# Performance work log

Measured on AMD Instinct MI355X. Metric: run time of the kernel, lower is better.

## Reference

```python
import jax, jax.numpy as jnp
import numpy as np

INPUT_DIM = 256
DEPTH = 8
HIDDEN = 64
NUM_INNER = 2 ** DEPTH - 1   # 255
NUM_LEAVES = 2 ** DEPTH      # 256
BATCH = 8192


def _xavier(key, shape, fan_in, fan_out):
    bound = jnp.sqrt(6.0 / (fan_in + fan_out)).astype(jnp.float32)
    return jax.random.uniform(key, shape, jnp.float32, -bound, bound)


def setup_inputs() -> dict:
    key = jax.random.key(0)
    k = jax.random.split(key, 5)
    x = jax.random.normal(k[0], (BATCH, INPUT_DIM), jnp.float32)
    # Batched per-node MLP params (one slice per inner node)
    w1 = _xavier(k[1], (NUM_INNER, HIDDEN, INPUT_DIM), INPUT_DIM, HIDDEN)
    b1 = jnp.zeros((NUM_INNER, HIDDEN), jnp.float32)
    w2 = _xavier(k[2], (NUM_INNER, HIDDEN), HIDDEN, 1)
    b2 = jnp.zeros((NUM_INNER,), jnp.float32)
    leaf = _xavier(k[3], (NUM_LEAVES, 1), NUM_LEAVES, 1)
    return {"x": x, "w1": w1, "b1": b1, "w2": w2, "b2": b2, "leaf": leaf}


def reference(x, w1, b1, w2, b2, leaf):
    B = x.shape[0]
    # Fused per-node MLPs: hidden [B, N, H]
    h = jax.nn.relu(jnp.einsum("bi,nhi->bnh", x, w1) + b1)
    logits = jnp.einsum("bnh,nh->bn", h, w2) + b2        # [B, N]
    node_outputs = jax.nn.sigmoid(logits)                 # p, in BFS node order

    # Tree traversal: level-by-level interleave. Child of node j at a level
    # are 2j (left, weight 1-p) and 2j+1 (right, weight p) at the next level.
    reach_levels = []
    cur = jnp.ones((B, 1), x.dtype)
    for level in range(DEPTH):
        reach_levels.append(cur)
        lo = (1 << level) - 1
        p_lvl = node_outputs[:, lo : lo + (1 << level)]   # [B, 2^level]
        cur = jnp.stack([cur * (1.0 - p_lvl), cur * p_lvl], axis=-1).reshape(B, -1)
    node_reach = jnp.concatenate(reach_levels, axis=1)    # [B, NUM_INNER], BFS order
    path_probs = cur                                      # [B, NUM_LEAVES]

    h_out = (path_probs @ leaf)[:, 0]                     # [B]
    return h_out, path_probs, node_outputs, node_reach
```

## Files before the change

kernel.cpp:

```cpp
#include <hip/hip_runtime.h>
#include <cstdint>

#define BATCH   8192
#define KDIM    256
#define HID     64
#define NODES   255
#define NPG     16

typedef unsigned short u16;
typedef unsigned int u32;
typedef short bf16x8 __attribute__((ext_vector_type(8)));
typedef float f32x16 __attribute__((ext_vector_type(16)));


__device__ __forceinline__ u32 f2bf(float f) {
  u32 u = __float_as_uint(f);
  return (u + 0x7FFFu + ((u >> 16) & 1u)) >> 16;
}

__device__ __forceinline__ void gld_lds16(const void* g, void* l) {
  typedef __attribute__((address_space(1))) void* gp_t;
  typedef __attribute__((address_space(3))) void* lp_t;
  gp_t gp = reinterpret_cast<gp_t>(reinterpret_cast<uintptr_t>(g));
  lp_t lp = reinterpret_cast<lp_t>(static_cast<u32>(reinterpret_cast<uintptr_t>(l)));
  __builtin_amdgcn_global_load_lds(gp, lp, 16, 0, 0);
}


#define NPRM 16320

__global__ __launch_bounds__(256) void cvt_kernel(
    const float* __restrict__ x, const float* __restrict__ w1,
    const float* __restrict__ b1, const float* __restrict__ w2,
    u16* __restrict__ xpack, u16* __restrict__ w1pk,
    float* __restrict__ b1p, float* __restrict__ w2p) {
  const int tid = threadIdx.x;
  const int blk = blockIdx.x;

  if (blk < 256) {
    __shared__ u16 sT[32 * 268];
    const float* xs = x + (size_t)blk * 32 * KDIM;
#pragma unroll
    for (int j = 0; j < 8; ++j) {
      int idx = j * 256 + tid;
      float4 v = ((const float4*)xs)[idx];
      int row = idx >> 6, f4 = idx & 63;
      *(u32*)&sT[row * 268 + f4 * 4]     = f2bf(v.x) | (f2bf(v.y) << 16);
      *(u32*)&sT[row * 268 + f4 * 4 + 2] = f2bf(v.z) | (f2bf(v.w) << 16);
    }
    __syncthreads();
#pragma unroll
    for (int j = 0; j < 4; ++j) {
      int d = j * 256 + tid;
      int ks = d >> 6, hl = (d >> 5) & 1, l31 = d & 31;
      const u16* s8 = &sT[l31 * 268 + ks * 16 + hl * 8];
      u32 a = *(const u32*)s8, b = *(const u32*)(s8 + 2);
      u32 c = *(const u32*)(s8 + 4), e = *(const u32*)(s8 + 6);
      uint4 o = {a, b, c, e};
      ((uint4*)xpack)[(size_t)blk * 1024 + d] = o;
    }
  } else if (blk < 511) {
    __shared__ u16 sT[64 * 260];
    const int node = blk - 256;
    const float* src = w1 + (size_t)node * (HID * KDIM);
#pragma unroll
    for (int r = 0; r < 16; ++r) {
      int idx = r * 256 + tid;
      float4 v = ((const float4*)src)[idx];
      int h = idx >> 6, f4 = idx & 63;
      uint2 o;
      o.x = f2bf(v.x) | (f2bf(v.y) << 16);
      o.y = f2bf(v.z) | (f2bf(v.w) << 16);
      *(uint2*)&sT[h * 260 + f4 * 4] = o;
    }
    __syncthreads();
    u16* dst = w1pk + (size_t)node * (HID * KDIM);
#pragma unroll
    for (int r = 0; r < 8; ++r) {
      int g = r * 256 + tid;
      int kb = g >> 6, h = g & 63;
      const u16* s8 = &sT[h * 260 + kb * 8];
      uint2 lo = *(const uint2*)s8;
      uint2 hi = *(const uint2*)(s8 + 4);
      uint4 o = {lo.x, lo.y, hi.x, hi.y};
      ((uint4*)dst)[g] = o;
    }
  } else {
    int i2 = (blk - 511) * 256 + tid;
    if (i2 < 2 * NPRM) {
      int a = i2 >= NPRM;
      int j = a ? i2 - NPRM : i2;
      int reg = j & 15, rt = (j >> 4) & 1, hl = (j >> 5) & 1, node = j >> 6;
      int h = rt * 32 + (reg & 3) + 8 * (reg >> 2) + 4 * hl;
      float v = (a ? b1 : w2)[node * 64 + h];
      (a ? b1p : w2p)[j] = v;
    }
  }
}


__global__ __launch_bounds__(256, 2) void fused_mlp_kernel(
    const u16* __restrict__ xpack,
    const u16* __restrict__ w1pk,
    const float* __restrict__ b1p,
    const float* __restrict__ w2p,
    const float* __restrict__ b2,
    float* __restrict__ no_t)
{
  __shared__ __align__(16) u16 sW[2][16384];
  __shared__ __align__(16) float sW2[NPG * 64];
  __shared__ __align__(16) float sB1[NPG * 64];
  __shared__ float sP[2][4][64];

  const int tid  = threadIdx.x;
  const int lane = tid & 63;
  const int wv   = tid >> 6;
  const int l31  = lane & 31;
  const int hl   = lane >> 5;
  const int rt   = wv & 1;
  const int ch   = wv >> 1;
  const int nbase = blockIdx.y * NPG;

  auto stage_node = [&](int nodeIdx, int bufIdx) {
    const u16* base = w1pk + (size_t)nodeIdx * (HID * KDIM);
    char* lb = (char*)(&sW[bufIdx][0]);
#pragma unroll
    for (int j = 0; j < 8; ++j) {
      int s = j * 256 + tid;
      gld_lds16(base + s * 8, lb + s * 16);
    }
  };

  stage_node(nbase, 0);
  gld_lds16(w2p + (size_t)nbase * 64 + tid * 4, (char*)sW2 + tid * 16);
  gld_lds16(b1p + (size_t)nbase * 64 + tid * 4, (char*)sB1 + tid * 16);

  const int ctile0 = blockIdx.x * 4 + ch * 2;
  bf16x8 xf[2][16];
#pragma unroll
  for (int ct = 0; ct < 2; ++ct) {
    const u16* src = xpack + ((size_t)(ctile0 + ct) * 16) * 512 + lane * 8;
#pragma unroll
    for (int ks = 0; ks < 16; ++ks)
      xf[ct][ks] = *(const bf16x8*)(src + ks * 512);
  }

  const u32 abase = (u32)(hl * 64 + rt * 32 + l31) * 16u;

  __syncthreads();
  int buf = 0, par = 0;

  for (int i = 0; i < NPG; ++i) {
    const int node = nbase + i;

    if (i + 1 < NPG) stage_node(nbase + i + 1, buf ^ 1);

    f32x16 acc0 = (f32x16){0}, acc1 = (f32x16){0};
    const char* sw = (const char*)&sW[buf][0] + abase;
#pragma unroll
    for (int ks = 0; ks < 16; ++ks) {
      bf16x8 a = *(const bf16x8*)(sw + ks * 2048);
      acc0 = __builtin_amdgcn_mfma_f32_32x32x16_bf16(a, xf[0][ks], acc0, 0, 0, 0);
      acc1 = __builtin_amdgcn_mfma_f32_32x32x16_bf16(a, xf[1][ks], acc1, 0, 0, 0);
    }

    float p0 = 0.f, p1 = 0.f;
#pragma unroll
    for (int qd = 0; qd < 4; ++qd) {
      int o = i * 64 + hl * 32 + rt * 16 + qd * 4;
      float4 wq = *(const float4*)&sW2[o];
      float4 bq = *(const float4*)&sB1[o];
#pragma unroll
      for (int e = 0; e < 4; ++e) {
        float w = (&wq.x)[e];
        float bb = (&bq.x)[e];
        p0 += fmaxf(acc0[qd * 4 + e] + bb, 0.f) * w;
        p1 += fmaxf(acc1[qd * 4 + e] + bb, 0.f) * w;
      }
    }
    p0 += __shfl_xor(p0, 32);
    p1 += __shfl_xor(p1, 32);
    if (hl == 0) {
      sP[par][wv][l31]      = p0;
      sP[par][wv][32 + l31] = p1;
    }

    __syncthreads();

    if (tid < 128 && node < NODES) {
      int chh = tid >> 6, c = tid & 63;
      float logit = sP[par][chh * 2][c] + sP[par][chh * 2 + 1][c] + b2[node];
      float sig = 1.0f / (1.0f + expf(-logit));
      no_t[(size_t)node * BATCH + blockIdx.x * 128 + tid] = sig;
    }

    buf ^= 1;
    par ^= 1;
  }
}


__global__ __launch_bounds__(256) void tree_kernel(
    const float* __restrict__ no_t,
    const float* __restrict__ leaf,
    float* __restrict__ out)
{
  __shared__ float p[16][257];

  const int tid = threadIdx.x;
  const int bbase = blockIdx.x * 16;
  const int wave = tid >> 6;
  const int lane = tid & 63;

  for (int i = tid; i < NODES * 16; i += 256) {
    int n = i >> 4, r = i & 15;
    p[r][n] = no_t[(size_t)n * BATCH + bbase + r];
  }
  __syncthreads();

  float4 lw = ((const float4*)leaf)[lane];

  float* h_out  = out;
  float* pp_out = out + 8192;
  float* no_out = out + 8192 + 8192 * 256;
  float* nr_out = out + 8192 + 8192 * 256 + 8192 * (size_t)NODES;

  for (int j = 0; j < 4; ++j) {
    const int r = wave * 4 + j;
    const int b = bbase + r;
    const float* pr = p[r];
    float* nr_b = nr_out + (size_t)b * NODES;

    float rc = 1.f;
#pragma unroll
    for (int L = 0; L < 6; ++L) {
      if (lane < (1 << L)) nr_b[(1 << L) - 1 + lane] = rc;
      float par = __shfl(rc, lane >> 1);
      float pv = pr[(1 << L) - 1 + (lane >> 1)];
      rc = par * ((lane & 1) ? pv : (1.f - pv));
    }
    nr_b[63 + lane] = rc;
    float p6 = pr[63 + lane];
    float r7a = rc * (1.f - p6), r7b = rc * p6;
    nr_b[127 + 2 * lane]     = r7a;
    nr_b[127 + 2 * lane + 1] = r7b;
    float p7a = pr[127 + 2 * lane], p7b = pr[127 + 2 * lane + 1];
    float4 pp;
    pp.x = r7a * (1.f - p7a);
    pp.y = r7a * p7a;
    pp.z = r7b * (1.f - p7b);
    pp.w = r7b * p7b;
    ((float4*)(pp_out + (size_t)b * 256))[lane] = pp;

    float* no_b = no_out + (size_t)b * NODES;
#pragma unroll
    for (int k = 0; k < 4; ++k) {
      int n = lane + 64 * k;
      if (n < NODES) no_b[n] = pr[n];
    }

    float hacc = pp.x * lw.x + pp.y * lw.y + pp.z * lw.z + pp.w * lw.w;
    hacc += __shfl_xor(hacc, 1);
    hacc += __shfl_xor(hacc, 2);
    hacc += __shfl_xor(hacc, 4);
    hacc += __shfl_xor(hacc, 8);
    hacc += __shfl_xor(hacc, 16);
    hacc += __shfl_xor(hacc, 32);
    if (lane == 0) h_out[b] = hacc;
  }
}


extern "C" void kernel_launch(void* const* d_in, const int* in_sizes, int n_in,
                              void* d_out, int out_size, void* d_ws, size_t ws_size,
                              hipStream_t stream) {
  const float* x    = (const float*)d_in[0];
  const float* w1   = (const float*)d_in[1];
  const float* b1   = (const float*)d_in[2];
  const float* w2   = (const float*)d_in[3];
  const float* b2   = (const float*)d_in[4];
  const float* leaf = (const float*)d_in[5];
  float* out = (float*)d_out;

  char* ws = (char*)d_ws;
  u16*   xpack = (u16*)ws;
  u16*   w1pk  = (u16*)(ws + (size_t)4194304);
  float* w2p   = (float*)(ws + (size_t)12582912);
  float* b1p   = (float*)(ws + (size_t)12648192);
  float* no_t  = (float*)(ws + (size_t)12713472);

  cvt_kernel<<<639, 256, 0, stream>>>(x, w1, b1, w2, xpack, w1pk, b1p, w2p);

  dim3 g(64, 16);
  fused_mlp_kernel<<<g, 256, 0, stream>>>(xpack, w1pk, b1p, w2p, b2, no_t);

  tree_kernel<<<BATCH / 16, 256, 0, stream>>>(no_t, leaf, out);
}
```

Measured before the change: 157.5 us.

## Compute full hidden dimension per wave and drop cross-wave LDS reduction

Each wave now computes all 64 hidden rows of a node for its own 64 batch columns, using four MFMA accumulators instead of two. Previously two waves each handled half the hidden rows and combined partial logits through shared memory. The change removes that LDS reduction and lets every thread write the sigmoid output directly. Each block now covers 256 batch rows, so the grid halves and each staged W1 tile is reused across twice as many columns. The cost is higher accumulator register pressure and half as many blocks to spread across the GPU.

```diff
diff --git a/kernel.cpp b/kernel.cpp
--- a/kernel.cpp
+++ b/kernel.cpp
@@ -110,15 +110,12 @@
   __shared__ __align__(16) u16 sW[2][16384];
   __shared__ __align__(16) float sW2[NPG * 64];
   __shared__ __align__(16) float sB1[NPG * 64];
-  __shared__ float sP[2][4][64];
 
   const int tid  = threadIdx.x;
   const int lane = tid & 63;
   const int wv   = tid >> 6;
   const int l31  = lane & 31;
   const int hl   = lane >> 5;
-  const int rt   = wv & 1;
-  const int ch   = wv >> 1;
   const int nbase = blockIdx.y * NPG;
 
   auto stage_node = [&](int nodeIdx, int bufIdx) {
@@ -135,7 +132,7 @@
   gld_lds16(w2p + (size_t)nbase * 64 + tid * 4, (char*)sW2 + tid * 16);
   gld_lds16(b1p + (size_t)nbase * 64 + tid * 4, (char*)sB1 + tid * 16);
 
-  const int ctile0 = blockIdx.x * 4 + ch * 2;
+  const int ctile0 = blockIdx.x * 8 + wv * 2;
   bf16x8 xf[2][16];
 #pragma unroll
   for (int ct = 0; ct < 2; ++ct) {
@@ -145,57 +142,61 @@
       xf[ct][ks] = *(const bf16x8*)(src + ks * 512);
   }
 
-  const u32 abase = (u32)(hl * 64 + rt * 32 + l31) * 16u;
+  const u32 abase = (u32)(hl * 64 + l31) * 16u;
 
   __syncthreads();
-  int buf = 0, par = 0;
+  int buf = 0;
 
   for (int i = 0; i < NPG; ++i) {
     const int node = nbase + i;
 
     if (i + 1 < NPG) stage_node(nbase + i + 1, buf ^ 1);
 
-    f32x16 acc0 = (f32x16){0}, acc1 = (f32x16){0};
+    f32x16 acc00 = (f32x16){0};
+    f32x16 acc01 = (f32x16){0};
+    f32x16 acc10 = (f32x16){0};
+    f32x16 acc11 = (f32x16){0};
     const char* sw = (const char*)&sW[buf][0] + abase;
 #pragma unroll
     for (int ks = 0; ks < 16; ++ks) {
-      bf16x8 a = *(const bf16x8*)(sw + ks * 2048);
-      acc0 = __builtin_amdgcn_mfma_f32_32x32x16_bf16(a, xf[0][ks], acc0, 0, 0, 0);
-      acc1 = __builtin_amdgcn_mfma_f32_32x32x16_bf16(a, xf[1][ks], acc1, 0, 0, 0);
+      bf16x8 a0 = *(const bf16x8*)(sw + ks * 2048);
+      bf16x8 a1 = *(const bf16x8*)(sw + ks * 2048 + 512);
+      acc00 = __builtin_amdgcn_mfma_f32_32x32x16_bf16(a0, xf[0][ks], acc00, 0, 0, 0);
+      acc01 = __builtin_amdgcn_mfma_f32_32x32x16_bf16(a0, xf[1][ks], acc01, 0, 0, 0);
+      acc10 = __builtin_amdgcn_mfma_f32_32x32x16_bf16(a1, xf[0][ks], acc10, 0, 0, 0);
+      acc11 = __builtin_amdgcn_mfma_f32_32x32x16_bf16(a1, xf[1][ks], acc11, 0, 0, 0);
     }
 
     float p0 = 0.f, p1 = 0.f;
 #pragma unroll
     for (int qd = 0; qd < 4; ++qd) {
-      int o = i * 64 + hl * 32 + rt * 16 + qd * 4;
-      float4 wq = *(const float4*)&sW2[o];
-      float4 bq = *(const float4*)&sB1[o];
+      int o = i * 64 + hl * 32 + qd * 4;
+      float4 w0 = *(const float4*)&sW2[o];
+      float4 b0 = *(const float4*)&sB1[o];
+      float4 w1q = *(const float4*)&sW2[o + 16];
+      float4 b1q = *(const float4*)&sB1[o + 16];
 #pragma unroll
       for (int e = 0; e < 4; ++e) {
-        float w = (&wq.x)[e];
-        float bb = (&bq.x)[e];
-        p0 += fmaxf(acc0[qd * 4 + e] + bb, 0.f) * w;
-        p1 += fmaxf(acc1[qd * 4 + e] + bb, 0.f) * w;
+        int r = qd * 4 + e;
+        float w0e = (&w0.x)[e], b0e = (&b0.x)[e];
+        float w1e = (&w1q.x)[e], b1e = (&b1q.x)[e];
+        p0 += fmaxf(acc00[r] + b0e, 0.f) * w0e;
+        p1 += fmaxf(acc01[r] + b0e, 0.f) * w0e;
+        p0 += fmaxf(acc10[r] + b1e, 0.f) * w1e;
+        p1 += fmaxf(acc11[r] + b1e, 0.f) * w1e;
       }
     }
     p0 += __shfl_xor(p0, 32);
     p1 += __shfl_xor(p1, 32);
-    if (hl == 0) {
-      sP[par][wv][l31]      = p0;
-      sP[par][wv][32 + l31] = p1;
+
+    if (node < NODES) {
+      float pv = hl ? p1 : p0;
+      float sig = 1.0f / (1.0f + expf(-(pv + b2[node])));
+      no_t[(size_t)node * BATCH + blockIdx.x * 256 + wv * 64 + lane] = sig;
     }
 
     __syncthreads();
-
-    if (tid < 128 && node < NODES) {
-      int chh = tid >> 6, c = tid & 63;
-      float logit = sP[par][chh * 2][c] + sP[par][chh * 2 + 1][c] + b2[node];
-      float sig = 1.0f / (1.0f + expf(-logit));
-      no_t[(size_t)node * BATCH + blockIdx.x * 128 + tid] = sig;
-    }
-
     buf ^= 1;
-    par ^= 1;
   }
 }
 
@@ -291,7 +292,7 @@
 
   cvt_kernel<<<639, 256, 0, stream>>>(x, w1, b1, w2, xpack, w1pk, b1p, w2p);
 
-  dim3 g(64, 16);
+  dim3 g(32, 16);
   fused_mlp_kernel<<<g, 256, 0, stream>>>(xpack, w1pk, b1p, w2p, b2, no_t);
 
   tree_kernel<<<BATCH / 16, 256, 0, stream>>>(no_t, leaf, out);
```

After: 152.8 us. 1.03x faster.

## Software-pipeline MLP epilogue into next node's MFMA loop, per-wave column tiles

Applied to the files above, without the earlier changes.

Each wave now owns one 32-column batch tile covering all 64 hidden units (two MFMAs sharing an x fragment), so the cross-wave LDS reduction through sP disappears. The ReLU/w2 epilogue for node i-1 is interleaved with node i's MFMA loop using double-buffered accumulators, overlapping VALU work with matrix work. w2 and b1 are packed into one interleaved float2 array, so a single LDS read gives both. The cost is more accumulator and register pressure, and x fragment reuse drops from two tiles to one per wave.

```diff
diff --git a/kernel.cpp b/kernel.cpp
--- a/kernel.cpp
+++ b/kernel.cpp
@@ -33,7 +33,7 @@
     const float* __restrict__ x, const float* __restrict__ w1,
     const float* __restrict__ b1, const float* __restrict__ w2,
     u16* __restrict__ xpack, u16* __restrict__ w1pk,
-    float* __restrict__ b1p, float* __restrict__ w2p) {
+    float2* __restrict__ wbp) {
   const int tid = threadIdx.x;
   const int blk = blockIdx.x;
 
@@ -86,14 +86,14 @@
       ((uint4*)dst)[g] = o;
     }
   } else {
-    int i2 = (blk - 511) * 256 + tid;
-    if (i2 < 2 * NPRM) {
-      int a = i2 >= NPRM;
-      int j = a ? i2 - NPRM : i2;
-      int reg = j & 15, rt = (j >> 4) & 1, hl = (j >> 5) & 1, node = j >> 6;
-      int h = rt * 32 + (reg & 3) + 8 * (reg >> 2) + 4 * hl;
-      float v = (a ? b1 : w2)[node * 64 + h];
-      (a ? b1p : w2p)[j] = v;
+    int j = (blk - 511) * 256 + tid;
+    if (j < NPRM) {
+      int reg = j & 15, ht = (j >> 4) & 1, hl = (j >> 5) & 1, node = j >> 6;
+      int h = ht * 32 + (reg & 3) + 8 * (reg >> 2) + 4 * hl;
+      float2 v;
+      v.x = w2[node * 64 + h];
+      v.y = b1[node * 64 + h];
+      wbp[j] = v;
     }
   }
 }
@@ -102,24 +102,20 @@
 __global__ __launch_bounds__(256, 2) void fused_mlp_kernel(
     const u16* __restrict__ xpack,
     const u16* __restrict__ w1pk,
-    const float* __restrict__ b1p,
-    const float* __restrict__ w2p,
+    const float2* __restrict__ wbp,
     const float* __restrict__ b2,
     float* __restrict__ no_t)
 {
   __shared__ __align__(16) u16 sW[2][16384];
-  __shared__ __align__(16) float sW2[NPG * 64];
-  __shared__ __align__(16) float sB1[NPG * 64];
-  __shared__ float sP[2][4][64];
+  __shared__ __align__(16) float2 sWB[NPG * 64];
 
   const int tid  = threadIdx.x;
   const int lane = tid & 63;
   const int wv   = tid >> 6;
   const int l31  = lane & 31;
   const int hl   = lane >> 5;
-  const int rt   = wv & 1;
-  const int ch   = wv >> 1;
   const int nbase = blockIdx.y * NPG;
+  const int colBase = blockIdx.x * 128 + wv * 32;
 
   auto stage_node = [&](int nodeIdx, int bufIdx) {
     const u16* base = w1pk + (size_t)nodeIdx * (HID * KDIM);
@@ -132,71 +128,94 @@
   };
 
   stage_node(nbase, 0);
-  gld_lds16(w2p + (size_t)nbase * 64 + tid * 4, (char*)sW2 + tid * 16);
-  gld_lds16(b1p + (size_t)nbase * 64 + tid * 4, (char*)sB1 + tid * 16);
-
-  const int ctile0 = blockIdx.x * 4 + ch * 2;
-  bf16x8 xf[2][16];
-#pragma unroll
-  for (int ct = 0; ct < 2; ++ct) {
-    const u16* src = xpack + ((size_t)(ctile0 + ct) * 16) * 512 + lane * 8;
+  {
+    const char* wsrc = (const char*)(wbp + (size_t)nbase * 64);
+    gld_lds16(wsrc + tid * 16,        (char*)sWB + tid * 16);
+    gld_lds16(wsrc + 4096 + tid * 16, (char*)sWB + 4096 + tid * 16);
+  }
+
+  const int ctile = blockIdx.x * 4 + wv;
+  bf16x8 xf[16];
+  {
+    const u16* src = xpack + (size_t)ctile * 8192 + lane * 8;
 #pragma unroll
     for (int ks = 0; ks < 16; ++ks)
-      xf[ct][ks] = *(const bf16x8*)(src + ks * 512);
-  }
-
-  const u32 abase = (u32)(hl * 64 + rt * 32 + l31) * 16u;
+      xf[ks] = *(const bf16x8*)(src + ks * 512);
+  }
+
+  const u32 abase = (u32)(hl * 64 + l31) * 16u;
+
+  f32x16 accA0, accA1, accB0, accB1;
 
   __syncthreads();
-  int buf = 0, par = 0;
-
-  for (int i = 0; i < NPG; ++i) {
-    const int node = nbase + i;
-
-    if (i + 1 < NPG) stage_node(nbase + i + 1, buf ^ 1);
-
-    f32x16 acc0 = (f32x16){0}, acc1 = (f32x16){0};
-    const char* sw = (const char*)&sW[buf][0] + abase;
+
+#define NODE_STEP(C0, C1, P0, P1, doEpi, iN)                                   \
+  {                                                                            \
+    if ((iN) + 1 < NPG) stage_node(nbase + (iN) + 1, ((iN) + 1) & 1);          \
+    C0 = (f32x16){0};                                                          \
+    C1 = (f32x16){0};                                                          \
+    const char* sw = (const char*)&sW[(iN) & 1][0] + abase;                    \
+    float pacc = 0.f;                                                          \
+    float4 wq0[8], wq1[8];                                                     \
+    if (doEpi) {                                                               \
+      const int wbo = ((iN) - 1) * 64 + hl * 32;                               \
+      _Pragma("unroll")                                                        \
+      for (int q = 0; q < 8; ++q) {                                            \
+        wq0[q] = *(const float4*)&sWB[wbo + 2 * q];                            \
+        wq1[q] = *(const float4*)&sWB[wbo + 16 + 2 * q];                       \
+      }                                                                        \
+    }                                                                          \
+    _Pragma("unroll")                                                          \
+    for (int ks = 0; ks < 16; ++ks) {                                          \
+      bf16x8 a0 = *(const bf16x8*)(sw + ks * 2048);                            \
+      bf16x8 a1 = *(const bf16x8*)(sw + ks * 2048 + 512);                      \
+      C0 = __builtin_amdgcn_mfma_f32_32x32x16_bf16(a0, xf[ks], C0, 0, 0, 0);   \
+      C1 = __builtin_amdgcn_mfma_f32_32x32x16_bf16(a1, xf[ks], C1, 0, 0, 0);   \
+      if (doEpi) {                                                             \
+        float4 q0 = wq0[ks >> 1], q1 = wq1[ks >> 1];                           \
+        float w0 = (ks & 1) ? q0.z : q0.x, b0 = (ks & 1) ? q0.w : q0.y;        \
+        float w1v = (ks & 1) ? q1.z : q1.x, b1v = (ks & 1) ? q1.w : q1.y;      \
+        pacc += fmaxf(P0[ks] + b0, 0.f) * w0;                                  \
+        pacc += fmaxf(P1[ks] + b1v, 0.f) * w1v;                                \
+      }                                                                        \
+    }                                                                          \
+    if (doEpi) {                                                               \
+      const int prvNode = nbase + (iN) - 1;                                    \
+      pacc += __shfl_xor(pacc, 32);                                            \
+      if (prvNode < NODES && hl == 0) {                                        \
+        float sig = 1.0f / (1.0f + expf(-(pacc + b2[prvNode])));               \
+        no_t[(size_t)prvNode * BATCH + colBase + l31] = sig;                   \
+      }                                                                        \
+    }                                                                          \
+    __syncthreads();                                                           \
+  }
+
+  NODE_STEP(accA0, accA1, accB0, accB1, false, 0);
+#pragma unroll
+  for (int ii = 1; ii <= 13; ii += 2) {
+    NODE_STEP(accB0, accB1, accA0, accA1, true, ii);
+    NODE_STEP(accA0, accA1, accB0, accB1, true, ii + 1);
+  }
+  NODE_STEP(accB0, accB1, accA0, accA1, true, 15);
+
+  {
+    const int node = nbase + 15;
+    float pacc = 0.f;
+    const int wbo = 15 * 64 + hl * 32;
 #pragma unroll
     for (int ks = 0; ks < 16; ++ks) {
-      bf16x8 a = *(const bf16x8*)(sw + ks * 2048);
-      acc0 = __builtin_amdgcn_mfma_f32_32x32x16_bf16(a, xf[0][ks], acc0, 0, 0, 0);
-      acc1 = __builtin_amdgcn_mfma_f32_32x32x16_bf16(a, xf[1][ks], acc1, 0, 0, 0);
-    }
-
-    float p0 = 0.f, p1 = 0.f;
-#pragma unroll
-    for (int qd = 0; qd < 4; ++qd) {
-      int o = i * 64 + hl * 32 + rt * 16 + qd * 4;
-      float4 wq = *(const float4*)&sW2[o];
-      float4 bq = *(const float4*)&sB1[o];
-#pragma unroll
-      for (int e = 0; e < 4; ++e) {
-        float w = (&wq.x)[e];
-        float bb = (&bq.x)[e];
-        p0 += fmaxf(acc0[qd * 4 + e] + bb, 0.f) * w;
-        p1 += fmaxf(acc1[qd * 4 + e] + bb, 0.f) * w;
-      }
-    }
-    p0 += __shfl_xor(p0, 32);
-    p1 += __shfl_xor(p1, 32);
-    if (hl == 0) {
-      sP[par][wv][l31]      = p0;
-      sP[par][wv][32 + l31] = p1;
-    }
-
-    __syncthreads();
-
-    if (tid < 128 && node < NODES) {
-      int chh = tid >> 6, c = tid & 63;
-      float logit = sP[par][chh * 2][c] + sP[par][chh * 2 + 1][c] + b2[node];
-      float sig = 1.0f / (1.0f + expf(-logit));
-      no_t[(size_t)node * BATCH + blockIdx.x * 128 + tid] = sig;
-    }
-
-    buf ^= 1;
-    par ^= 1;
-  }
+      float2 wb0 = sWB[wbo + ks];
+      float2 wb1 = sWB[wbo + 16 + ks];
+      pacc += fmaxf(accB0[ks] + wb0.y, 0.f) * wb0.x;
+      pacc += fmaxf(accB1[ks] + wb1.y, 0.f) * wb1.x;
+    }
+    pacc += __shfl_xor(pacc, 32);
+    if (node < NODES && hl == 0) {
+      float sig = 1.0f / (1.0f + expf(-(pacc + b2[node])));
+      no_t[(size_t)node * BATCH + colBase + l31] = sig;
+    }
+  }
+#undef NODE_STEP
 }
 
 
@@ -283,16 +302,15 @@
   float* out = (float*)d_out;
 
   char* ws = (char*)d_ws;
-  u16*   xpack = (u16*)ws;
-  u16*   w1pk  = (u16*)(ws + (size_t)4194304);
-  float* w2p   = (float*)(ws + (size_t)12582912);
-  float* b1p   = (float*)(ws + (size_t)12648192);
-  float* no_t  = (float*)(ws + (size_t)12713472);
-
-  cvt_kernel<<<639, 256, 0, stream>>>(x, w1, b1, w2, xpack, w1pk, b1p, w2p);
+  u16*    xpack = (u16*)ws;
+  u16*    w1pk  = (u16*)(ws + (size_t)4194304);
+  float2* wbp   = (float2*)(ws + (size_t)12582912);
+  float*  no_t  = (float*)(ws + (size_t)12713472);
+
+  cvt_kernel<<<575, 256, 0, stream>>>(x, w1, b1, w2, xpack, w1pk, wbp);
 
   dim3 g(64, 16);
-  fused_mlp_kernel<<<g, 256, 0, stream>>>(xpack, w1pk, b1p, w2p, b2, no_t);
+  fused_mlp_kernel<<<g, 256, 0, stream>>>(xpack, w1pk, wbp, b2, no_t);
 
   tree_kernel<<<BATCH / 16, 256, 0, stream>>>(no_t, leaf, out);
 }
```

Result: no change. 158.6 us (+0.7%).
